# Kernel optimization log

Hardware: AMD Instinct MI355X
Metric: run time of the kernel (lower is better)

## Reference

```python
import jax, jax.numpy as jnp
import numpy as np

N_NODES = 50000


def _gcn_conv(h, src, dst, W, b, n_nodes):
    """PyG GCNConv: add self-loops, symmetric deg^{-1/2} normalization,
    linear transform, scatter-add aggregation at target nodes."""
    h = h @ W  # [N, out]
    # self-loops
    loop = jnp.arange(n_nodes, dtype=src.dtype)
    s = jnp.concatenate([src, loop])  # source j
    d = jnp.concatenate([dst, loop])  # target i
    ones = jnp.ones(s.shape[0], dtype=h.dtype)
    deg = jax.ops.segment_sum(ones, d, num_segments=n_nodes)  # in-degree incl. self-loop
    dinv = jnp.where(deg > 0, jax.lax.rsqrt(deg), 0.0)
    norm = dinv[s] * dinv[d]  # [E+N]
    msg = h[s] * norm[:, None]  # gather + scale, [E+N, out]
    out = jax.ops.segment_sum(msg, d, num_segments=n_nodes)  # scatter-add
    return out + b


def reference(x, edge_index, q_emb, W1, b1, W2, b2, Wq, bq):
    src, dst = edge_index[0], edge_index[1]
    n = x.shape[0]
    # dropout rates are 0.0 -> identity
    h1 = jax.nn.relu(_gcn_conv(x, src, dst, W1, b1, n))
    h2 = _gcn_conv(h1, src, dst, W2, b2, n)
    ques = q_emb @ Wq + bq
    return (ques, h2)


def setup_inputs() -> dict:
    key = jax.random.key(0)
    ks = jax.random.split(key, 9)
    d = 128
    sc = 1.0 / np.sqrt(d)
    return {
        "x": jax.random.normal(ks[0], (N_NODES, d), dtype=jnp.float32),
        "edge_index": jax.random.randint(ks[1], (2, 800000), 0, N_NODES, dtype=jnp.int64),
        "q_emb": jax.random.normal(ks[2], (20000, d), dtype=jnp.float32),
        "W1": jax.random.normal(ks[3], (d, d), dtype=jnp.float32) * sc,
        "b1": jax.random.normal(ks[4], (d,), dtype=jnp.float32) * 0.01,
        "W2": jax.random.normal(ks[5], (d, d), dtype=jnp.float32) * sc,
        "b2": jax.random.normal(ks[6], (d,), dtype=jnp.float32) * 0.01,
        "Wq": jax.random.normal(ks[7], (d, d), dtype=jnp.float32) * sc,
        "bq": jax.random.normal(ks[8], (d,), dtype=jnp.float32) * 0.01,
    }
```

## Files before the change

kernel.cpp:

```cpp
#include <hip/hip_runtime.h>

#define D 128
#define NFB 256
#define CAP 64

typedef __attribute__((ext_vector_type(8))) short bf16x8;
typedef __attribute__((ext_vector_type(4))) float f32x4;

__device__ __forceinline__ unsigned short f2b(float v) {
    unsigned u = __float_as_uint(v);
    unsigned r = u + 0x7fffu + ((u >> 16) & 1u);
    return (unsigned short)(r >> 16);
}
__device__ __forceinline__ float b2f(unsigned short h) {
    return __uint_as_float(((unsigned)h) << 16);
}


__global__ __launch_bounds__(256) void prep(int* __restrict__ cnt, int N, int nbz,
                                            const float* __restrict__ W1,
                                            const float* __restrict__ W2,
                                            const float* __restrict__ Wq,
                                            unsigned short* __restrict__ o1,
                                            unsigned short* __restrict__ o2,
                                            unsigned short* __restrict__ oq) {
    int b = blockIdx.x;
    if (b < nbz) {
        int idx = b * 256 + threadIdx.x;
        if (idx * 4 + 4 <= N) {
            ((int4*)cnt)[idx] = make_int4(0, 0, 0, 0);
        } else {
            for (int k = idx * 4; k < N; ++k) cnt[k] = 0;
        }
        return;
    }
    int t = (b - nbz) * 256 + threadIdx.x;
    int which = t >> 14;
    int r = t & 16383;
    int n = r >> 7, k = r & 127;
    const float* W = (which == 0) ? W1 : (which == 1) ? W2 : Wq;
    unsigned short* o = (which == 0) ? o1 : (which == 1) ? o2 : oq;
    o[r] = f2b(W[k * D + n]);
}


__device__ __forceinline__ void gemm_body(const float* Af,
                                          const unsigned short* __restrict__ Wth,
                                          const float* bias, unsigned short* Cb,
                                          float* Cf, int M, int bid, int outf,
                                          char* smem) {
    int lane = threadIdx.x & 63;
    int wave = threadIdx.x >> 6;
    int m16 = (bid * 4 + wave) * 16;
    if (m16 >= M) return;
    int mrow = lane & 15;
    int quad = lane >> 4;

    f32x4 acc[8];
#pragma unroll
    for (int nt = 0; nt < 8; ++nt) acc[nt] = (f32x4){0.f, 0.f, 0.f, 0.f};

    int arow = m16 + mrow;

#pragma unroll
    for (int ks = 0; ks < 4; ++ks) {
        bf16x8 ah, al;
        const float* ap = Af + (size_t)arow * D + ks * 32 + quad * 8;
        float4 v0 = *(const float4*)ap;
        float4 v1 = *(const float4*)(ap + 4);
        float vv[8] = {v0.x, v0.y, v0.z, v0.w, v1.x, v1.y, v1.z, v1.w};
#pragma unroll
        for (int j = 0; j < 8; ++j) {
            unsigned short h = f2b(vv[j]);
            ah[j] = (short)h;
            al[j] = (short)f2b(vv[j] - b2f(h));
        }
#pragma unroll
        for (int nt = 0; nt < 8; ++nt) {
            bf16x8 wf = *(const bf16x8*)(Wth + (size_t)(nt * 16 + mrow) * D + ks * 32 + quad * 8);
            acc[nt] = __builtin_amdgcn_mfma_f32_16x16x32_bf16(ah, wf, acc[nt], 0, 0, 0);
            acc[nt] = __builtin_amdgcn_mfma_f32_16x16x32_bf16(al, wf, acc[nt], 0, 0, 0);
        }
    }

    if (outf == 0) {
        unsigned short* myl = (unsigned short*)smem + wave * 16 * 136;
#pragma unroll
        for (int nt = 0; nt < 8; ++nt) {
            int col = nt * 16 + mrow;
#pragma unroll
            for (int r = 0; r < 4; ++r)
                myl[(quad * 4 + r) * 136 + col] = f2b(acc[nt][r]);
        }
#pragma unroll
        for (int R = 0; R < 16; ++R) {
            unsigned int v = *(const unsigned int*)&myl[R * 136 + lane * 2];
            ((unsigned int*)(Cb + (size_t)(m16 + R) * D))[lane] = v;
        }
    } else {
#pragma unroll
        for (int nt = 0; nt < 8; ++nt) {
            int col = nt * 16 + mrow;
            float bv = bias[col];
#pragma unroll
            for (int r = 0; r < 4; ++r)
                Cf[(size_t)(m16 + quad * 4 + r) * D + col] = acc[nt][r] + bv;
        }
    }
}

__global__ __launch_bounds__(256) void frontfill(const float* __restrict__ x,
                                                 const float* __restrict__ q,
                                                 const unsigned short* __restrict__ Wth1,
                                                 const unsigned short* __restrict__ Wthq,
                                                 const float* __restrict__ bq,
                                                 unsigned short* __restrict__ Cb,
                                                 float* __restrict__ outq,
                                                 const int* __restrict__ src,
                                                 const int* __restrict__ dst,
                                                 int* __restrict__ cnt,
                                                 int* __restrict__ colv,
                                                 int N, int MQ, int E, int nbN) {
    __shared__ char smem[4 * 16 * 136 * 2];
    int b = blockIdx.x;
    if (b < NFB) {
        const int4* d4 = (const int4*)dst;
        const int4* s4 = (const int4*)src;
        int n4 = E >> 2;
        int stride = NFB * 256;
        for (int idx = b * 256 + threadIdx.x; idx < n4; idx += stride) {
            int4 dv = d4[idx];
            int4 sv = s4[idx];
            int slot;
            slot = atomicAdd(&cnt[dv.x], 1);
            if (slot < CAP) colv[(size_t)dv.x * CAP + slot] = sv.x;
            slot = atomicAdd(&cnt[dv.y], 1);
            if (slot < CAP) colv[(size_t)dv.y * CAP + slot] = sv.y;
            slot = atomicAdd(&cnt[dv.z], 1);
            if (slot < CAP) colv[(size_t)dv.z * CAP + slot] = sv.z;
            slot = atomicAdd(&cnt[dv.w], 1);
            if (slot < CAP) colv[(size_t)dv.w * CAP + slot] = sv.w;
        }
        for (int e = (n4 << 2) + b * 256 + threadIdx.x; e < E; e += stride) {
            int d = dst[e];
            int slot = atomicAdd(&cnt[d], 1);
            if (slot < CAP) colv[(size_t)d * CAP + slot] = src[e];
        }
        return;
    }
    b -= NFB;
    if (b < nbN)
        gemm_body(x, Wth1, nullptr, Cb, nullptr, N, b, 0, smem);
    else
        gemm_body(q, Wthq, bq, nullptr, outq, MQ, b - nbN, 1, smem);
}

__device__ __forceinline__ void agg_node(const bf16x8* __restrict__ T8,
                                         const int* __restrict__ colv,
                                         const int* __restrict__ cnt,
                                         int i, int lane, int g, int l16,
                                         float acc[8]) {
#pragma unroll
    for (int k = 0; k < 8; ++k) acc[k] = 0.f;
    int deg = cnt[i];
    int ci = (deg < CAP) ? deg : CAP;
    int e0 = i * CAP;
    int e1 = e0 + ci;
    for (int base = e0; base < e1; base += 64) {
        int cb = e1 - base;
        if (cb > 64) cb = 64;
        int jv = 0;
        float wv = 0.f;
        if (lane < cb) {
            jv = colv[base + lane];
            wv = rsqrtf((float)(cnt[jv] + 1));
        }
        int t = 0;
        for (; t + 16 <= cb; t += 16) {
            int j0 = __shfl(jv, t + g);
            int j1 = __shfl(jv, t + 4 + g);
            int j2 = __shfl(jv, t + 8 + g);
            int j3 = __shfl(jv, t + 12 + g);
            float w0 = __shfl(wv, t + g);
            float w1 = __shfl(wv, t + 4 + g);
            float w2 = __shfl(wv, t + 8 + g);
            float w3 = __shfl(wv, t + 12 + g);
            bf16x8 r0 = T8[(size_t)j0 * 16 + l16];
            bf16x8 r1 = T8[(size_t)j1 * 16 + l16];
            bf16x8 r2 = T8[(size_t)j2 * 16 + l16];
            bf16x8 r3 = T8[(size_t)j3 * 16 + l16];
#pragma unroll
            for (int k = 0; k < 8; ++k) acc[k] = fmaf(w0, b2f((unsigned short)r0[k]), acc[k]);
#pragma unroll
            for (int k = 0; k < 8; ++k) acc[k] = fmaf(w1, b2f((unsigned short)r1[k]), acc[k]);
#pragma unroll
            for (int k = 0; k < 8; ++k) acc[k] = fmaf(w2, b2f((unsigned short)r2[k]), acc[k]);
#pragma unroll
            for (int k = 0; k < 8; ++k) acc[k] = fmaf(w3, b2f((unsigned short)r3[k]), acc[k]);
        }
        for (; t < cb; t += 4) {
            int j = __shfl(jv, t + g);
            float w = __shfl(wv, t + g);
            if (w > 0.f) {
                bf16x8 r = T8[(size_t)j * 16 + l16];
#pragma unroll
                for (int k = 0; k < 8; ++k) acc[k] = fmaf(w, b2f((unsigned short)r[k]), acc[k]);
            }
        }
    }
#pragma unroll
    for (int k = 0; k < 8; ++k) {
        acc[k] += __shfl_xor(acc[k], 16);
        acc[k] += __shfl_xor(acc[k], 32);
    }
}

__global__ __launch_bounds__(512) void agg1_gemm(const unsigned short* __restrict__ Tb,
                                                 const int* __restrict__ colv,
                                                 const int* __restrict__ cnt,
                                                 const float* __restrict__ bias,
                                                 const unsigned short* __restrict__ Wth2,
                                                 unsigned short* __restrict__ Cb2,
                                                 int N) {
    __shared__ unsigned short AH[16 * 136];
    __shared__ unsigned short AL[16 * 136];
    int wave = threadIdx.x >> 6;
    int lane = threadIdx.x & 63;
    int g = lane >> 4;
    int l16 = lane & 15;
    int node0 = blockIdx.x * 16;
    const bf16x8* T8 = (const bf16x8*)Tb;

#pragma unroll
    for (int sub = 0; sub < 2; ++sub) {
        int row = wave * 2 + sub;
        int i = node0 + row;
        float acc[8];
        if (i < N) {
            agg_node(T8, colv, cnt, i, lane, g, l16, acc);
            if (g == 0) {
                int deg = cnt[i];
                float di = rsqrtf((float)(deg + 1));
                bf16x8 selfr = T8[(size_t)i * 16 + l16];
                float4 b0 = ((const float4*)bias)[l16 * 2];
                float4 b1v = ((const float4*)bias)[l16 * 2 + 1];
                float bb[8] = {b0.x, b0.y, b0.z, b0.w, b1v.x, b1v.y, b1v.z, b1v.w};
                bf16x8 h, l;
#pragma unroll
                for (int k = 0; k < 8; ++k) {
                    float r = di * acc[k] + di * di * b2f((unsigned short)selfr[k]) + bb[k];
                    r = fmaxf(r, 0.f);
                    unsigned short hh = f2b(r);
                    h[k] = (short)hh;
                    l[k] = (short)f2b(r - b2f(hh));
                }
                *(bf16x8*)&AH[row * 136 + l16 * 8] = h;
                *(bf16x8*)&AL[row * 136 + l16 * 8] = l;
            }
        } else if (g == 0) {
            bf16x8 z = (bf16x8){0, 0, 0, 0, 0, 0, 0, 0};
            *(bf16x8*)&AH[row * 136 + l16 * 8] = z;
            *(bf16x8*)&AL[row * 136 + l16 * 8] = z;
        }
    }
    __syncthreads();

    int nt = wave;
    int mrow = l16;
    int quad = g;
    f32x4 acc2 = (f32x4){0.f, 0.f, 0.f, 0.f};
#pragma unroll
    for (int ks = 0; ks < 4; ++ks) {
        bf16x8 ah = *(const bf16x8*)&AH[mrow * 136 + ks * 32 + quad * 8];
        bf16x8 al = *(const bf16x8*)&AL[mrow * 136 + ks * 32 + quad * 8];
        bf16x8 wf = *(const bf16x8*)(Wth2 + (size_t)(nt * 16 + mrow) * D + ks * 32 + quad * 8);
        acc2 = __builtin_amdgcn_mfma_f32_16x16x32_bf16(ah, wf, acc2, 0, 0, 0);
        acc2 = __builtin_amdgcn_mfma_f32_16x16x32_bf16(al, wf, acc2, 0, 0, 0);
    }
    __syncthreads();
    {
        int col = nt * 16 + mrow;
#pragma unroll
        for (int r = 0; r < 4; ++r) {
            int gi = node0 + quad * 4 + r;
            float dr = (gi < N) ? rsqrtf((float)(cnt[gi] + 1)) : 0.f;
            AH[(quad * 4 + r) * 136 + col] = f2b(acc2[r] * dr);
        }
    }
    __syncthreads();
#pragma unroll
    for (int k = 0; k < 2; ++k) {
        int idx = threadIdx.x + k * 512;
        int row = idx >> 6;
        int c = idx & 63;
        if (node0 + row < N) {
            unsigned int v = *(const unsigned int*)&AH[row * 136 + c * 2];
            ((unsigned int*)(Cb2 + (size_t)(node0 + row) * D))[c] = v;
        }
    }
}

__global__ __launch_bounds__(512) void aggregate2(const unsigned short* __restrict__ Tb,
                                                  const int* __restrict__ colv,
                                                  const int* __restrict__ cnt,
                                                  const float* __restrict__ bias,
                                                  float* __restrict__ Of, int N) {
    int wave = threadIdx.x >> 6;
    int lane = threadIdx.x & 63;
    int i = blockIdx.x * 8 + wave;
    if (i >= N) return;
    int g = lane >> 4;
    int l16 = lane & 15;
    const bf16x8* T8 = (const bf16x8*)Tb;

    float acc[8];
#pragma unroll
    for (int k = 0; k < 8; ++k) acc[k] = 0.f;

    int deg = cnt[i];
    int ci = (deg < CAP) ? deg : CAP;
    int e0 = i * CAP;
    int e1 = e0 + ci;
    for (int base = e0; base < e1; base += 64) {
        int cb = e1 - base;
        if (cb > 64) cb = 64;
        int jv = (lane < cb) ? colv[base + lane] : 0;
        int t = 0;
        for (; t + 16 <= cb; t += 16) {
            int j0 = __shfl(jv, t + g);
            int j1 = __shfl(jv, t + 4 + g);
            int j2 = __shfl(jv, t + 8 + g);
            int j3 = __shfl(jv, t + 12 + g);
            bf16x8 r0 = T8[(size_t)j0 * 16 + l16];
            bf16x8 r1 = T8[(size_t)j1 * 16 + l16];
            bf16x8 r2 = T8[(size_t)j2 * 16 + l16];
            bf16x8 r3 = T8[(size_t)j3 * 16 + l16];
#pragma unroll
            for (int k = 0; k < 8; ++k)
                acc[k] += b2f((unsigned short)r0[k]) + b2f((unsigned short)r1[k]) +
                          b2f((unsigned short)r2[k]) + b2f((unsigned short)r3[k]);
        }
        for (; t < cb; t += 4) {
            int j = __shfl(jv, t + g);
            if (t + g < cb) {
                bf16x8 r = T8[(size_t)j * 16 + l16];
#pragma unroll
                for (int k = 0; k < 8; ++k) acc[k] += b2f((unsigned short)r[k]);
            }
        }
    }

#pragma unroll
    for (int k = 0; k < 8; ++k) {
        acc[k] += __shfl_xor(acc[k], 16);
        acc[k] += __shfl_xor(acc[k], 32);
    }

    if (g == 0) {
        float di = rsqrtf((float)(deg + 1));
        bf16x8 selfr = T8[(size_t)i * 16 + l16];
        float4 b0 = ((const float4*)bias)[l16 * 2];
        float4 b1v = ((const float4*)bias)[l16 * 2 + 1];
        float bb[8] = {b0.x, b0.y, b0.z, b0.w, b1v.x, b1v.y, b1v.z, b1v.w};
        float4 r0, r1;
        r0.x = di * (acc[0] + b2f((unsigned short)selfr[0])) + bb[0];
        r0.y = di * (acc[1] + b2f((unsigned short)selfr[1])) + bb[1];
        r0.z = di * (acc[2] + b2f((unsigned short)selfr[2])) + bb[2];
        r0.w = di * (acc[3] + b2f((unsigned short)selfr[3])) + bb[3];
        r1.x = di * (acc[4] + b2f((unsigned short)selfr[4])) + bb[4];
        r1.y = di * (acc[5] + b2f((unsigned short)selfr[5])) + bb[5];
        r1.z = di * (acc[6] + b2f((unsigned short)selfr[6])) + bb[6];
        r1.w = di * (acc[7] + b2f((unsigned short)selfr[7])) + bb[7];
        ((float4*)Of)[(size_t)i * 32 + l16 * 2] = r0;
        ((float4*)Of)[(size_t)i * 32 + l16 * 2 + 1] = r1;
    }
}


static inline char* carve(char*& w, size_t bytes) {
    char* p = w;
    w += (bytes + 255) & ~(size_t)255;
    return p;
}

extern "C" void kernel_launch(void* const* d_in, const int* in_sizes, int n_in,
                              void* d_out, int out_size, void* d_ws, size_t ws_size,
                              hipStream_t stream) {
    const float* x  = (const float*)d_in[0];
    const int*   ei = (const int*)d_in[1];
    const float* q  = (const float*)d_in[2];
    const float* W1 = (const float*)d_in[3];
    const float* b1 = (const float*)d_in[4];
    const float* W2 = (const float*)d_in[5];
    const float* b2 = (const float*)d_in[6];
    const float* Wq = (const float*)d_in[7];
    const float* bq = (const float*)d_in[8];

    int N  = in_sizes[0] / D;
    int E  = in_sizes[1] / 2;
    int MQ = in_sizes[2] / D;

    const int* srcv = ei;
    const int* dstv = ei + E;

    char* w = (char*)d_ws;
    unsigned short* Cb   = (unsigned short*)carve(w, (size_t)N * D * 2);
    unsigned short* Cb2  = (unsigned short*)carve(w, (size_t)N * D * 2);
    int*            colv = (int*)carve(w, (size_t)N * CAP * 4);
    int*            cnt  = (int*)carve(w, (size_t)N * 4);
    unsigned short* Wth1 = (unsigned short*)carve(w, D * D * 2);
    unsigned short* Wth2 = (unsigned short*)carve(w, D * D * 2);
    unsigned short* Wthq = (unsigned short*)carve(w, D * D * 2);

    float* outq = (float*)d_out;
    float* outh = outq + (size_t)MQ * D;

    int nbz = (N / 4 + 255) / 256;
    int nbN = (N + 63) / 64;
    int nbQ = (MQ + 63) / 64;

    prep<<<nbz + 192, 256, 0, stream>>>(cnt, N, nbz, W1, W2, Wq, Wth1, Wth2, Wthq);
    frontfill<<<NFB + nbN + nbQ, 256, 0, stream>>>(x, q, Wth1, Wthq, bq, Cb, outq,
                                                   srcv, dstv, cnt, colv,
                                                   N, MQ, E, nbN);
    agg1_gemm<<<(N + 15) / 16, 512, 0, stream>>>(Cb, colv, cnt, b1, Wth2, Cb2, N);
    aggregate2<<<(N + 7) / 8, 512, 0, stream>>>(Cb2, colv, cnt, b2, outh, N);
}
```

Measured before the change: 236.6 us.

## Pad degree counters to separate cache lines and precompute dinv array

```diff
diff --git a/kernel.cpp b/kernel.cpp
--- a/kernel.cpp
+++ b/kernel.cpp
@@ -1,7 +1,7 @@
 #include <hip/hip_runtime.h>
 
 #define D 128
-#define NFB 256
+#define NFB 512
 #define CAP 64
 
 typedef __attribute__((ext_vector_type(8))) short bf16x8;
@@ -17,7 +17,7 @@
 }
 
 
-__global__ __launch_bounds__(256) void prep(int* __restrict__ cnt, int N, int nbz,
+__global__ __launch_bounds__(256) void prep(int* __restrict__ cnt_s, int N16, int nbz,
                                             const float* __restrict__ W1,
                                             const float* __restrict__ W2,
                                             const float* __restrict__ Wq,
@@ -27,10 +27,10 @@
     int b = blockIdx.x;
     if (b < nbz) {
         int idx = b * 256 + threadIdx.x;
-        if (idx * 4 + 4 <= N) {
-            ((int4*)cnt)[idx] = make_int4(0, 0, 0, 0);
+        if (idx * 4 + 4 <= N16) {
+            ((int4*)cnt_s)[idx] = make_int4(0, 0, 0, 0);
         } else {
-            for (int k = idx * 4; k < N; ++k) cnt[k] = 0;
+            for (int k = idx * 4; k < N16; ++k) cnt_s[k] = 0;
         }
         return;
     }
@@ -41,6 +41,17 @@
     const float* W = (which == 0) ? W1 : (which == 1) ? W2 : Wq;
     unsigned short* o = (which == 0) ? o1 : (which == 1) ? o2 : oq;
     o[r] = f2b(W[k * D + n]);
+}
+
+__global__ __launch_bounds__(256) void compact(const int* __restrict__ cnt_s,
+                                               int* __restrict__ cnt,
+                                               float* __restrict__ dinv, int N) {
+    int i = blockIdx.x * 256 + threadIdx.x;
+    if (i < N) {
+        int d = cnt_s[i << 4];
+        cnt[i] = d;
+        dinv[i] = rsqrtf((float)(d + 1));
+    }
 }
 
 
@@ -118,7 +129,7 @@
                                                  float* __restrict__ outq,
                                                  const int* __restrict__ src,
                                                  const int* __restrict__ dst,
-                                                 int* __restrict__ cnt,
+                                                 int* __restrict__ cnt_s,
                                                  int* __restrict__ colv,
                                                  int N, int MQ, int E, int nbN) {
     __shared__ char smem[4 * 16 * 136 * 2];
@@ -132,18 +143,18 @@
             int4 dv = d4[idx];
             int4 sv = s4[idx];
             int slot;
-            slot = atomicAdd(&cnt[dv.x], 1);
+            slot = atomicAdd(&cnt_s[dv.x << 4], 1);
             if (slot < CAP) colv[(size_t)dv.x * CAP + slot] = sv.x;
-            slot = atomicAdd(&cnt[dv.y], 1);
+            slot = atomicAdd(&cnt_s[dv.y << 4], 1);
             if (slot < CAP) colv[(size_t)dv.y * CAP + slot] = sv.y;
-            slot = atomicAdd(&cnt[dv.z], 1);
+            slot = atomicAdd(&cnt_s[dv.z << 4], 1);
             if (slot < CAP) colv[(size_t)dv.z * CAP + slot] = sv.z;
-            slot = atomicAdd(&cnt[dv.w], 1);
+            slot = atomicAdd(&cnt_s[dv.w << 4], 1);
             if (slot < CAP) colv[(size_t)dv.w * CAP + slot] = sv.w;
         }
         for (int e = (n4 << 2) + b * 256 + threadIdx.x; e < E; e += stride) {
             int d = dst[e];
-            int slot = atomicAdd(&cnt[d], 1);
+            int slot = atomicAdd(&cnt_s[d << 4], 1);
             if (slot < CAP) colv[(size_t)d * CAP + slot] = src[e];
         }
         return;
@@ -158,6 +169,7 @@
 __device__ __forceinline__ void agg_node(const bf16x8* __restrict__ T8,
                                          const int* __restrict__ colv,
                                          const int* __restrict__ cnt,
+                                         const float* __restrict__ dinv,
                                          int i, int lane, int g, int l16,
                                          float acc[8]) {
 #pragma unroll
@@ -173,7 +185,7 @@
         float wv = 0.f;
         if (lane < cb) {
             jv = colv[base + lane];
-            wv = rsqrtf((float)(cnt[jv] + 1));
+            wv = dinv[jv];
         }
         int t = 0;
         for (; t + 16 <= cb; t += 16) {
@@ -218,6 +230,7 @@
 __global__ __launch_bounds__(512) void agg1_gemm(const unsigned short* __restrict__ Tb,
                                                  const int* __restrict__ colv,
                                                  const int* __restrict__ cnt,
+                                                 const float* __restrict__ dinv,
                                                  const float* __restrict__ bias,
                                                  const unsigned short* __restrict__ Wth2,
                                                  unsigned short* __restrict__ Cb2,
@@ -237,10 +250,9 @@
         int i = node0 + row;
         float acc[8];
         if (i < N) {
-            agg_node(T8, colv, cnt, i, lane, g, l16, acc);
+            agg_node(T8, colv, cnt, dinv, i, lane, g, l16, acc);
             if (g == 0) {
-                int deg = cnt[i];
-                float di = rsqrtf((float)(deg + 1));
+                float di = dinv[i];
                 bf16x8 selfr = T8[(size_t)i * 16 + l16];
                 float4 b0 = ((const float4*)bias)[l16 * 2];
                 float4 b1v = ((const float4*)bias)[l16 * 2 + 1];
@@ -283,7 +295,7 @@
 #pragma unroll
         for (int r = 0; r < 4; ++r) {
             int gi = node0 + quad * 4 + r;
-            float dr = (gi < N) ? rsqrtf((float)(cnt[gi] + 1)) : 0.f;
+            float dr = (gi < N) ? dinv[gi] : 0.f;
             AH[(quad * 4 + r) * 136 + col] = f2b(acc2[r] * dr);
         }
     }
@@ -303,6 +315,7 @@
 __global__ __launch_bounds__(512) void aggregate2(const unsigned short* __restrict__ Tb,
                                                   const int* __restrict__ colv,
                                                   const int* __restrict__ cnt,
+                                                  const float* __restrict__ dinv,
                                                   const float* __restrict__ bias,
                                                   float* __restrict__ Of, int N) {
     int wave = threadIdx.x >> 6;
@@ -357,7 +370,7 @@
     }
 
     if (g == 0) {
-        float di = rsqrtf((float)(deg + 1));
+        float di = dinv[i];
         bf16x8 selfr = T8[(size_t)i * 16 + l16];
         float4 b0 = ((const float4*)bias)[l16 * 2];
         float4 b1v = ((const float4*)bias)[l16 * 2 + 1];
@@ -404,25 +417,29 @@
     const int* dstv = ei + E;
 
     char* w = (char*)d_ws;
-    unsigned short* Cb   = (unsigned short*)carve(w, (size_t)N * D * 2);
-    unsigned short* Cb2  = (unsigned short*)carve(w, (size_t)N * D * 2);
-    int*            colv = (int*)carve(w, (size_t)N * CAP * 4);
-    int*            cnt  = (int*)carve(w, (size_t)N * 4);
-    unsigned short* Wth1 = (unsigned short*)carve(w, D * D * 2);
-    unsigned short* Wth2 = (unsigned short*)carve(w, D * D * 2);
-    unsigned short* Wthq = (unsigned short*)carve(w, D * D * 2);
+    unsigned short* Cb    = (unsigned short*)carve(w, (size_t)N * D * 2);
+    unsigned short* Cb2   = (unsigned short*)carve(w, (size_t)N * D * 2);
+    int*            colv  = (int*)carve(w, (size_t)N * CAP * 4);
+    int*            cnt_s = (int*)carve(w, (size_t)N * 16 * 4);
+    int*            cnt   = (int*)carve(w, (size_t)N * 4);
+    float*          dinv  = (float*)carve(w, (size_t)N * 4);
+    unsigned short* Wth1  = (unsigned short*)carve(w, D * D * 2);
+    unsigned short* Wth2  = (unsigned short*)carve(w, D * D * 2);
+    unsigned short* Wthq  = (unsigned short*)carve(w, D * D * 2);
 
     float* outq = (float*)d_out;
     float* outh = outq + (size_t)MQ * D;
 
-    int nbz = (N / 4 + 255) / 256;
+    int N16 = N * 16;
+    int nbz = (N16 / 4 + 255) / 256;
     int nbN = (N + 63) / 64;
     int nbQ = (MQ + 63) / 64;
 
-    prep<<<nbz + 192, 256, 0, stream>>>(cnt, N, nbz, W1, W2, Wq, Wth1, Wth2, Wthq);
+    prep<<<nbz + 192, 256, 0, stream>>>(cnt_s, N16, nbz, W1, W2, Wq, Wth1, Wth2, Wthq);
     frontfill<<<NFB + nbN + nbQ, 256, 0, stream>>>(x, q, Wth1, Wthq, bq, Cb, outq,
-                                                   srcv, dstv, cnt, colv,
+                                                   srcv, dstv, cnt_s, colv,
                                                    N, MQ, E, nbN);
-    agg1_gemm<<<(N + 15) / 16, 512, 0, stream>>>(Cb, colv, cnt, b1, Wth2, Cb2, N);
-    aggregate2<<<(N + 7) / 8, 512, 0, stream>>>(Cb2, colv, cnt, b2, outh, N);
-}
+    compact<<<(N + 255) / 256, 256, 0, stream>>>(cnt_s, cnt, dinv, N);
+    agg1_gemm<<<(N + 15) / 16, 512, 0, stream>>>(Cb, colv, cnt, dinv, b1, Wth2, Cb2, N);
+    aggregate2<<<(N + 7) / 8, 512, 0, stream>>>(Cb2, colv, cnt, dinv, b2, outh, N);
+}
```

Result: slower. 243.5 us (+2.9%).

## Split edge-fill from GEMM kernel, memset counts, simplify aggregation loops

Applied to the files above, without the earlier changes.

```diff
diff --git a/kernel.cpp b/kernel.cpp
--- a/kernel.cpp
+++ b/kernel.cpp
@@ -1,7 +1,7 @@
 #include <hip/hip_runtime.h>
 
 #define D 128
-#define NFB 256
+#define NFB 768
 #define CAP 64
 
 typedef __attribute__((ext_vector_type(8))) short bf16x8;
@@ -16,31 +16,49 @@
     return __uint_as_float(((unsigned)h) << 16);
 }
 
-
-__global__ __launch_bounds__(256) void prep(int* __restrict__ cnt, int N, int nbz,
-                                            const float* __restrict__ W1,
-                                            const float* __restrict__ W2,
-                                            const float* __restrict__ Wq,
-                                            unsigned short* __restrict__ o1,
-                                            unsigned short* __restrict__ o2,
-                                            unsigned short* __restrict__ oq) {
+__global__ __launch_bounds__(256) void fillw(const int* __restrict__ src,
+                                             const int* __restrict__ dst,
+                                             int* __restrict__ cnt,
+                                             int* __restrict__ colv, int E,
+                                             const float* __restrict__ W1,
+                                             const float* __restrict__ W2,
+                                             const float* __restrict__ Wq,
+                                             unsigned short* __restrict__ o1,
+                                             unsigned short* __restrict__ o2,
+                                             unsigned short* __restrict__ oq) {
     int b = blockIdx.x;
-    if (b < nbz) {
-        int idx = b * 256 + threadIdx.x;
-        if (idx * 4 + 4 <= N) {
-            ((int4*)cnt)[idx] = make_int4(0, 0, 0, 0);
-        } else {
-            for (int k = idx * 4; k < N; ++k) cnt[k] = 0;
-        }
+    if (b >= NFB) {
+        int t = (b - NFB) * 256 + threadIdx.x;
+        int which = t >> 14;
+        int r = t & 16383;
+        int n = r >> 7, k = r & 127;
+        const float* W = (which == 0) ? W1 : (which == 1) ? W2 : Wq;
+        unsigned short* o = (which == 0) ? o1 : (which == 1) ? o2 : oq;
+        o[r] = f2b(W[k * D + n]);
         return;
     }
-    int t = (b - nbz) * 256 + threadIdx.x;
-    int which = t >> 14;
-    int r = t & 16383;
-    int n = r >> 7, k = r & 127;
-    const float* W = (which == 0) ? W1 : (which == 1) ? W2 : Wq;
-    unsigned short* o = (which == 0) ? o1 : (which == 1) ? o2 : oq;
-    o[r] = f2b(W[k * D + n]);
+    const int4* d4 = (const int4*)dst;
+    const int4* s4 = (const int4*)src;
+    int n4 = E >> 2;
+    int stride = NFB * 256;
+    for (int idx = b * 256 + threadIdx.x; idx < n4; idx += stride) {
+        int4 dv = d4[idx];
+        int4 sv = s4[idx];
+        int slot;
+        slot = atomicAdd(&cnt[dv.x], 1);
+        if (slot < CAP) colv[(size_t)dv.x * CAP + slot] = sv.x;
+        slot = atomicAdd(&cnt[dv.y], 1);
+        if (slot < CAP) colv[(size_t)dv.y * CAP + slot] = sv.y;
+        slot = atomicAdd(&cnt[dv.z], 1);
+        if (slot < CAP) colv[(size_t)dv.z * CAP + slot] = sv.z;
+        slot = atomicAdd(&cnt[dv.w], 1);
+        if (slot < CAP) colv[(size_t)dv.w * CAP + slot] = sv.w;
+    }
+    for (int e = (n4 << 2) + b * 256 + threadIdx.x; e < E; e += stride) {
+        int d = dst[e];
+        int slot = atomicAdd(&cnt[d], 1);
+        if (slot < CAP) colv[(size_t)d * CAP + slot] = src[e];
+    }
 }
 
 
@@ -109,46 +127,16 @@
     }
 }
 
-__global__ __launch_bounds__(256) void frontfill(const float* __restrict__ x,
-                                                 const float* __restrict__ q,
-                                                 const unsigned short* __restrict__ Wth1,
-                                                 const unsigned short* __restrict__ Wthq,
-                                                 const float* __restrict__ bq,
-                                                 unsigned short* __restrict__ Cb,
-                                                 float* __restrict__ outq,
-                                                 const int* __restrict__ src,
-                                                 const int* __restrict__ dst,
-                                                 int* __restrict__ cnt,
-                                                 int* __restrict__ colv,
-                                                 int N, int MQ, int E, int nbN) {
+__global__ __launch_bounds__(256) void gemm1q(const float* __restrict__ x,
+                                              const float* __restrict__ q,
+                                              const unsigned short* __restrict__ Wth1,
+                                              const unsigned short* __restrict__ Wthq,
+                                              const float* __restrict__ bq,
+                                              unsigned short* __restrict__ Cb,
+                                              float* __restrict__ outq,
+                                              int N, int MQ, int nbN) {
     __shared__ char smem[4 * 16 * 136 * 2];
     int b = blockIdx.x;
-    if (b < NFB) {
-        const int4* d4 = (const int4*)dst;
-        const int4* s4 = (const int4*)src;
-        int n4 = E >> 2;
-        int stride = NFB * 256;
-        for (int idx = b * 256 + threadIdx.x; idx < n4; idx += stride) {
-            int4 dv = d4[idx];
-            int4 sv = s4[idx];
-            int slot;
-            slot = atomicAdd(&cnt[dv.x], 1);
-            if (slot < CAP) colv[(size_t)dv.x * CAP + slot] = sv.x;
-            slot = atomicAdd(&cnt[dv.y], 1);
-            if (slot < CAP) colv[(size_t)dv.y * CAP + slot] = sv.y;
-            slot = atomicAdd(&cnt[dv.z], 1);
-            if (slot < CAP) colv[(size_t)dv.z * CAP + slot] = sv.z;
-            slot = atomicAdd(&cnt[dv.w], 1);
-            if (slot < CAP) colv[(size_t)dv.w * CAP + slot] = sv.w;
-        }
-        for (int e = (n4 << 2) + b * 256 + threadIdx.x; e < E; e += stride) {
-            int d = dst[e];
-            int slot = atomicAdd(&cnt[d], 1);
-            if (slot < CAP) colv[(size_t)d * CAP + slot] = src[e];
-        }
-        return;
-    }
-    b -= NFB;
     if (b < nbN)
         gemm_body(x, Wth1, nullptr, Cb, nullptr, N, b, 0, smem);
     else
@@ -158,54 +146,46 @@
 __device__ __forceinline__ void agg_node(const bf16x8* __restrict__ T8,
                                          const int* __restrict__ colv,
                                          const int* __restrict__ cnt,
-                                         int i, int lane, int g, int l16,
+                                         int i, int ci, int lane, int g, int l16,
                                          float acc[8]) {
 #pragma unroll
     for (int k = 0; k < 8; ++k) acc[k] = 0.f;
-    int deg = cnt[i];
-    int ci = (deg < CAP) ? deg : CAP;
-    int e0 = i * CAP;
-    int e1 = e0 + ci;
-    for (int base = e0; base < e1; base += 64) {
-        int cb = e1 - base;
-        if (cb > 64) cb = 64;
-        int jv = 0;
-        float wv = 0.f;
-        if (lane < cb) {
-            jv = colv[base + lane];
-            wv = rsqrtf((float)(cnt[jv] + 1));
-        }
-        int t = 0;
-        for (; t + 16 <= cb; t += 16) {
-            int j0 = __shfl(jv, t + g);
-            int j1 = __shfl(jv, t + 4 + g);
-            int j2 = __shfl(jv, t + 8 + g);
-            int j3 = __shfl(jv, t + 12 + g);
-            float w0 = __shfl(wv, t + g);
-            float w1 = __shfl(wv, t + 4 + g);
-            float w2 = __shfl(wv, t + 8 + g);
-            float w3 = __shfl(wv, t + 12 + g);
-            bf16x8 r0 = T8[(size_t)j0 * 16 + l16];
-            bf16x8 r1 = T8[(size_t)j1 * 16 + l16];
-            bf16x8 r2 = T8[(size_t)j2 * 16 + l16];
-            bf16x8 r3 = T8[(size_t)j3 * 16 + l16];
-#pragma unroll
-            for (int k = 0; k < 8; ++k) acc[k] = fmaf(w0, b2f((unsigned short)r0[k]), acc[k]);
-#pragma unroll
-            for (int k = 0; k < 8; ++k) acc[k] = fmaf(w1, b2f((unsigned short)r1[k]), acc[k]);
-#pragma unroll
-            for (int k = 0; k < 8; ++k) acc[k] = fmaf(w2, b2f((unsigned short)r2[k]), acc[k]);
-#pragma unroll
-            for (int k = 0; k < 8; ++k) acc[k] = fmaf(w3, b2f((unsigned short)r3[k]), acc[k]);
-        }
-        for (; t < cb; t += 4) {
-            int j = __shfl(jv, t + g);
-            float w = __shfl(wv, t + g);
-            if (w > 0.f) {
-                bf16x8 r = T8[(size_t)j * 16 + l16];
-#pragma unroll
-                for (int k = 0; k < 8; ++k) acc[k] = fmaf(w, b2f((unsigned short)r[k]), acc[k]);
-            }
+    int jv = 0;
+    float wv = 0.f;
+    if (lane < ci) {
+        jv = colv[i * CAP + lane];
+        wv = rsqrtf((float)(cnt[jv] + 1));
+    }
+    int t = 0;
+    for (; t + 16 <= ci; t += 16) {
+        int j0 = __shfl(jv, t + g);
+        int j1 = __shfl(jv, t + 4 + g);
+        int j2 = __shfl(jv, t + 8 + g);
+        int j3 = __shfl(jv, t + 12 + g);
+        float w0 = __shfl(wv, t + g);
+        float w1 = __shfl(wv, t + 4 + g);
+        float w2 = __shfl(wv, t + 8 + g);
+        float w3 = __shfl(wv, t + 12 + g);
+        bf16x8 r0 = T8[(size_t)j0 * 16 + l16];
+        bf16x8 r1 = T8[(size_t)j1 * 16 + l16];
+        bf16x8 r2 = T8[(size_t)j2 * 16 + l16];
+        bf16x8 r3 = T8[(size_t)j3 * 16 + l16];
+#pragma unroll
+        for (int k = 0; k < 8; ++k) acc[k] = fmaf(w0, b2f((unsigned short)r0[k]), acc[k]);
+#pragma unroll
+        for (int k = 0; k < 8; ++k) acc[k] = fmaf(w1, b2f((unsigned short)r1[k]), acc[k]);
+#pragma unroll
+        for (int k = 0; k < 8; ++k) acc[k] = fmaf(w2, b2f((unsigned short)r2[k]), acc[k]);
+#pragma unroll
+        for (int k = 0; k < 8; ++k) acc[k] = fmaf(w3, b2f((unsigned short)r3[k]), acc[k]);
+    }
+    for (; t < ci; t += 4) {
+        int j = __shfl(jv, t + g);
+        float w = __shfl(wv, t + g);
+        if (w > 0.f) {
+            bf16x8 r = T8[(size_t)j * 16 + l16];
+#pragma unroll
+            for (int k = 0; k < 8; ++k) acc[k] = fmaf(w, b2f((unsigned short)r[k]), acc[k]);
         }
     }
 #pragma unroll
@@ -237,9 +217,10 @@
         int i = node0 + row;
         float acc[8];
         if (i < N) {
-            agg_node(T8, colv, cnt, i, lane, g, l16, acc);
+            int deg = cnt[i];
+            int ci = (deg < CAP) ? deg : CAP;
+            agg_node(T8, colv, cnt, i, ci, lane, g, l16, acc);
             if (g == 0) {
-                int deg = cnt[i];
                 float di = rsqrtf((float)(deg + 1));
                 bf16x8 selfr = T8[(size_t)i * 16 + l16];
                 float4 b0 = ((const float4*)bias)[l16 * 2];
@@ -313,40 +294,38 @@
     int l16 = lane & 15;
     const bf16x8* T8 = (const bf16x8*)Tb;
 
-    float acc[8];
-#pragma unroll
-    for (int k = 0; k < 8; ++k) acc[k] = 0.f;
-
     int deg = cnt[i];
     int ci = (deg < CAP) ? deg : CAP;
-    int e0 = i * CAP;
-    int e1 = e0 + ci;
-    for (int base = e0; base < e1; base += 64) {
-        int cb = e1 - base;
-        if (cb > 64) cb = 64;
-        int jv = (lane < cb) ? colv[base + lane] : 0;
-        int t = 0;
-        for (; t + 16 <= cb; t += 16) {
-            int j0 = __shfl(jv, t + g);
-            int j1 = __shfl(jv, t + 4 + g);
-            int j2 = __shfl(jv, t + 8 + g);
-            int j3 = __shfl(jv, t + 12 + g);
-            bf16x8 r0 = T8[(size_t)j0 * 16 + l16];
-            bf16x8 r1 = T8[(size_t)j1 * 16 + l16];
-            bf16x8 r2 = T8[(size_t)j2 * 16 + l16];
-            bf16x8 r3 = T8[(size_t)j3 * 16 + l16];
-#pragma unroll
-            for (int k = 0; k < 8; ++k)
-                acc[k] += b2f((unsigned short)r0[k]) + b2f((unsigned short)r1[k]) +
-                          b2f((unsigned short)r2[k]) + b2f((unsigned short)r3[k]);
-        }
-        for (; t < cb; t += 4) {
-            int j = __shfl(jv, t + g);
-            if (t + g < cb) {
-                bf16x8 r = T8[(size_t)j * 16 + l16];
-#pragma unroll
-                for (int k = 0; k < 8; ++k) acc[k] += b2f((unsigned short)r[k]);
-            }
+    bf16x8 selfr = T8[(size_t)i * 16 + l16];
+    float4 b0 = ((const float4*)bias)[l16 * 2];
+    float4 b1v = ((const float4*)bias)[l16 * 2 + 1];
+
+    float acc[8];
+#pragma unroll
+    for (int k = 0; k < 8; ++k) acc[k] = 0.f;
+
+    int jv = (lane < ci) ? colv[i * CAP + lane] : 0;
+    int t = 0;
+    for (; t + 16 <= ci; t += 16) {
+        int j0 = __shfl(jv, t + g);
+        int j1 = __shfl(jv, t + 4 + g);
+        int j2 = __shfl(jv, t + 8 + g);
+        int j3 = __shfl(jv, t + 12 + g);
+        bf16x8 r0 = T8[(size_t)j0 * 16 + l16];
+        bf16x8 r1 = T8[(size_t)j1 * 16 + l16];
+        bf16x8 r2 = T8[(size_t)j2 * 16 + l16];
+        bf16x8 r3 = T8[(size_t)j3 * 16 + l16];
+#pragma unroll
+        for (int k = 0; k < 8; ++k)
+            acc[k] += b2f((unsigned short)r0[k]) + b2f((unsigned short)r1[k]) +
+                      b2f((unsigned short)r2[k]) + b2f((unsigned short)r3[k]);
+    }
+    for (; t < ci; t += 4) {
+        int j = __shfl(jv, t + g);
+        if (t + g < ci) {
+            bf16x8 r = T8[(size_t)j * 16 + l16];
+#pragma unroll
+            for (int k = 0; k < 8; ++k) acc[k] += b2f((unsigned short)r[k]);
         }
     }
 
@@ -358,9 +337,6 @@
 
     if (g == 0) {
         float di = rsqrtf((float)(deg + 1));
-        bf16x8 selfr = T8[(size_t)i * 16 + l16];
-        float4 b0 = ((const float4*)bias)[l16 * 2];
-        float4 b1v = ((const float4*)bias)[l16 * 2 + 1];
         float bb[8] = {b0.x, b0.y, b0.z, b0.w, b1v.x, b1v.y, b1v.z, b1v.w};
         float4 r0, r1;
         r0.x = di * (acc[0] + b2f((unsigned short)selfr[0])) + bb[0];
@@ -415,14 +391,13 @@
     float* outq = (float*)d_out;
     float* outh = outq + (size_t)MQ * D;
 
-    int nbz = (N / 4 + 255) / 256;
     int nbN = (N + 63) / 64;
     int nbQ = (MQ + 63) / 64;
 
-    prep<<<nbz + 192, 256, 0, stream>>>(cnt, N, nbz, W1, W2, Wq, Wth1, Wth2, Wthq);
-    frontfill<<<NFB + nbN + nbQ, 256, 0, stream>>>(x, q, Wth1, Wthq, bq, Cb, outq,
-                                                   srcv, dstv, cnt, colv,
-                                                   N, MQ, E, nbN);
+    hipMemsetAsync(cnt, 0, (size_t)N * 4, stream);
+    fillw<<<NFB + 192, 256, 0, stream>>>(srcv, dstv, cnt, colv, E,
+                                         W1, W2, Wq, Wth1, Wth2, Wthq);
+    gemm1q<<<nbN + nbQ, 256, 0, stream>>>(x, q, Wth1, Wthq, bq, Cb, outq, N, MQ, nbN);
     agg1_gemm<<<(N + 15) / 16, 512, 0, stream>>>(Cb, colv, cnt, b1, Wth2, Cb2, N);
     aggregate2<<<(N + 7) / 8, 512, 0, stream>>>(Cb2, colv, cnt, b2, outh, N);
 }
```

Result: slower. 249.6 us (+5.5%).
